# Performance work log

Hardware: AMD Instinct MI355X
Metric: run time of the kernel (lower is better)

Reference implementation:

```python
import jax, jax.numpy as jnp
import numpy as np

SEQ_LEN = 4096
HID = 2048      # hidden_dim == input_dim
NF = 512        # n_features


def setup_inputs() -> dict:
    key = jax.random.key(0)
    ks = jax.random.split(key, 13)
    s = 0.02
    return {
        "x": jax.random.normal(ks[0], (1, 1, NF), jnp.float32),
        "input_hidden": jax.random.normal(ks[1], (1, 1, HID), jnp.float32),
        "input_cell": jax.random.normal(ks[2], (1, 1, HID), jnp.float32),
        "encoder_outputs": jax.random.normal(ks[3], (1, SEQ_LEN, HID), jnp.float32),
        # Bahdanau attention params: Linear(2H -> H) and scoring vector v
        "W_attn": jax.random.normal(ks[4], (HID, 2 * HID), jnp.float32) * s,
        "b_attn": jnp.zeros((HID,), jnp.float32),
        "v_attn": jax.random.normal(ks[5], (HID,), jnp.float32) * s,
        # LSTM params (PyTorch layout, gate order i,f,g,o), input size = H + NF
        "W_ih": jax.random.normal(ks[6], (4 * HID, HID + NF), jnp.float32) * s,
        "W_hh": jax.random.normal(ks[7], (4 * HID, HID), jnp.float32) * s,
        "b_ih": jnp.zeros((4 * HID,), jnp.float32),
        "b_hh": jnp.zeros((4 * HID,), jnp.float32),
        # output Linear(2H -> NF)
        "W_out": jax.random.normal(ks[8], (NF, 2 * HID), jnp.float32) * s,
        "b_out": jnp.zeros((NF,), jnp.float32),
    }


def reference(x, input_hidden, input_cell, encoder_outputs,
              W_attn, b_attn, v_attn, W_ih, W_hh, b_ih, b_hh, W_out, b_out):
    # ---- attention(input_hidden, encoder_outputs) -> a: [B, S] ----
    h_last = input_hidden[-1]                      # [B, H]
    B, S, H = encoder_outputs.shape
    h_rep = jnp.broadcast_to(h_last[:, None, :], (B, S, H))
    energy = jnp.tanh(jnp.concatenate([h_rep, encoder_outputs], axis=-1) @ W_attn.T + b_attn)
    scores = jnp.einsum('bsh,h->bs', energy, v_attn)
    a = jax.nn.softmax(scores, axis=1)             # [B, S]

    # weighted = bmm(a.unsqueeze(1), encoder_outputs) -> [B, H]
    weighted = jnp.einsum('bs,bsh->bh', a, encoder_outputs)

    # ---- single-step LSTM (num_layers=1, batch_first) ----
    rnn_in = jnp.concatenate([x.reshape(1, -1), weighted], axis=-1)  # [1, NF+H]
    h0 = input_hidden[0]                           # [1, H]
    c0 = input_cell[0]                             # [1, H]
    gates = rnn_in @ W_ih.T + b_ih + h0 @ W_hh.T + b_hh  # [1, 4H]
    i, f, g, o = jnp.split(gates, 4, axis=-1)
    c_n = jax.nn.sigmoid(f) * c0 + jax.nn.sigmoid(i) * jnp.tanh(g)
    h_n = jax.nn.sigmoid(o) * jnp.tanh(c_n)        # [1, H] == output.squeeze(0)

    # ---- output projection on cat(output, weighted) ----
    out = jnp.concatenate([h_n, weighted], axis=-1) @ W_out.T + b_out  # [1, NF]
    return out, h_n[None], c_n[None]
```

## Files before the change

kernel.cpp:

```cpp
#include <hip/hip_runtime.h>
#include <hip/hip_bf16.h>
#include <math.h>


#define HIDDEN 2048
#define SEQL   4096
#define NFEAT  512

typedef __attribute__((ext_vector_type(8))) short frag_t;
typedef __attribute__((ext_vector_type(8))) unsigned short u16x8;
typedef __attribute__((ext_vector_type(4))) float f32x4;

__device__ __forceinline__ unsigned short f2bf(float f) {
    union { float f; unsigned int u; } c; c.f = f;
    unsigned int r = c.u + 0x7fffu + ((c.u >> 16) & 1u);
    return (unsigned short)(r >> 16);
}

__device__ __forceinline__ float bf2f(unsigned short u) {
    union { unsigned int u; float f; } c; c.u = (unsigned int)u << 16;
    return c.f;
}

__device__ __forceinline__ float wave_sum(float s) {
    #pragma unroll
    for (int off = 32; off; off >>= 1) s += __shfl_down(s, off);
    return s;
}

__device__ __forceinline__ void gload16(const unsigned short* g, unsigned short* l) {
    __builtin_amdgcn_global_load_lds(
        (const __attribute__((address_space(1))) unsigned int*)g,
        (__attribute__((address_space(3))) unsigned int*)l, 16, 0, 0);
}

__global__ __launch_bounds__(256)
void k_conv_hpre(const float* __restrict__ enc, const float* __restrict__ Wattn,
                 const float* __restrict__ b_attn, const float* __restrict__ h0,
                 unsigned short* __restrict__ encbf, unsigned short* __restrict__ wbf,
                 float* __restrict__ h_pre)
{
    const int b = blockIdx.x;
    if (b < 6144) {
        const float* src;
        unsigned short* dst;
        if (b < 4096) {
            src = enc + (size_t)b * 2048;
            dst = encbf + (size_t)b * 2048;
        } else {
            const int r = b - 4096;
            src = Wattn + (size_t)r * 4096 + 2048;
            dst = wbf + (size_t)r * 2048;
        }
        const int t = threadIdx.x;
        float4 a = *reinterpret_cast<const float4*>(src + t * 8);
        float4 c = *reinterpret_cast<const float4*>(src + t * 8 + 4);
        u16x8 o;
        o[0] = f2bf(a.x); o[1] = f2bf(a.y); o[2] = f2bf(a.z); o[3] = f2bf(a.w);
        o[4] = f2bf(c.x); o[5] = f2bf(c.y); o[6] = f2bf(c.z); o[7] = f2bf(c.w);
        *reinterpret_cast<u16x8*>(dst + t * 8) = o;
    } else {
        const int gw = (b - 6144) * 4 + (threadIdx.x >> 6);
        const int lane = threadIdx.x & 63;
        const float* Wr = Wattn + (size_t)gw * 4096;
        float s = 0.f;
        #pragma unroll
        for (int i = 0; i < 8; i++) {
            int c = i * 256 + lane * 4;
            float4 wv = *reinterpret_cast<const float4*>(Wr + c);
            float4 hv = *reinterpret_cast<const float4*>(h0 + c);
            s += wv.x*hv.x + wv.y*hv.y + wv.z*hv.z + wv.w*hv.w;
        }
        s = wave_sum(s);
        if (lane == 0) h_pre[gw] = s + b_attn[gw];
    }
}

__global__ __launch_bounds__(256)
void k_energy_gates(const unsigned short* __restrict__ encbf,
                    const unsigned short* __restrict__ wbf,
                    const float* __restrict__ h_pre, const float* __restrict__ v_attn,
                    const float* __restrict__ Wih,  const float* __restrict__ Whh,
                    const float* __restrict__ b_ih, const float* __restrict__ b_hh,
                    const float* __restrict__ x,    const float* __restrict__ h0,
                    float* __restrict__ pscore, float* __restrict__ gates)
{
    __shared__ __align__(16) unsigned short As[128 * 64];
    __shared__ __align__(16) unsigned short Bs[128 * 64];
    __shared__ float sh_hv[2][128];
    __shared__ float sh_part[2][128];

    const int tid = threadIdx.x;
    const int wv = tid >> 6, lane = tid & 63;

    if (blockIdx.x >= 512) {
        const int g = blockIdx.x - 512;
        #pragma unroll
        for (int r = 0; r < 2; r++) {
            const int j = g * 8 + wv * 2 + r;
            const float* W1 = Wih + (size_t)j * 2560;
            const float* W2 = Whh + (size_t)j * 2048;
            float s = 0.f;
            #pragma unroll
            for (int i = 0; i < 2; i++) {
                int c = i * 256 + lane * 4;
                float4 wvv = *reinterpret_cast<const float4*>(W1 + c);
                float4 xv = *reinterpret_cast<const float4*>(x + c);
                s += wvv.x*xv.x + wvv.y*xv.y + wvv.z*xv.z + wvv.w*xv.w;
            }
            #pragma unroll
            for (int i = 0; i < 8; i++) {
                int c = i * 256 + lane * 4;
                float4 wvv = *reinterpret_cast<const float4*>(W2 + c);
                float4 hv = *reinterpret_cast<const float4*>(h0 + c);
                s += wvv.x*hv.x + wvv.y*hv.y + wvv.z*hv.z + wvv.w*hv.w;
            }
            s = wave_sum(s);
            if (lane == 0) gates[j] = s + b_ih[j] + b_hh[j];
        }
        return;
    }

    const int hb = blockIdx.x & 15;
    const int sb = blockIdx.x >> 4;
    const int s0 = sb * 128, h0i = hb * 128;
    const int wm = wv >> 1, wn = wv & 1;

    const unsigned short* srcA[4];
    const unsigned short* srcB[4];
    #pragma unroll
    for (int i = 0; i < 4; i++) {
        const int c = wv * 4 + i;
        const int row = c * 8 + (lane >> 3);
        const int k0 = ((lane & 7) ^ (row & 7)) * 8;
        srcA[i] = encbf + (size_t)(s0 + row) * 2048 + k0;
        srcB[i] = wbf  + (size_t)(h0i + row) * 2048 + k0;
    }

    f32x4 acc[4][4];
    #pragma unroll
    for (int m = 0; m < 4; m++)
        #pragma unroll
        for (int n = 0; n < 4; n++)
            acc[m][n] = (f32x4){0.f, 0.f, 0.f, 0.f};

    const int swz = (lane & 7) << 4;
    const int hi16 = (lane >> 4) * 16;

    for (int kt = 0; kt < 2048; kt += 64) {
        __syncthreads();
        #pragma unroll
        for (int i = 0; i < 4; i++) {
            const int c = wv * 4 + i;
            gload16(srcA[i] + kt, &As[c * 512]);
            gload16(srcB[i] + kt, &Bs[c * 512]);
        }
        __syncthreads();

        frag_t af[2][4], bq[2][4];
        #pragma unroll
        for (int ks = 0; ks < 2; ks++) {
            const int lo = (ks * 64 + hi16) ^ swz;
            #pragma unroll
            for (int m = 0; m < 4; m++) {
                const int rowa = wm * 64 + m * 16 + (lane & 15);
                af[ks][m] = *reinterpret_cast<const frag_t*>(
                    reinterpret_cast<const char*>(As) + rowa * 128 + lo);
                const int rowb = wn * 64 + m * 16 + (lane & 15);
                bq[ks][m] = *reinterpret_cast<const frag_t*>(
                    reinterpret_cast<const char*>(Bs) + rowb * 128 + lo);
            }
        }
        #pragma unroll
        for (int ks = 0; ks < 2; ks++)
            #pragma unroll
            for (int m = 0; m < 4; m++)
                #pragma unroll
                for (int n = 0; n < 4; n++)
                    acc[m][n] = __builtin_amdgcn_mfma_f32_16x16x32_bf16(
                        af[ks][m], bq[ks][n], acc[m][n], 0, 0, 0);
    }

    if (tid < 128) { sh_hv[0][tid] = h_pre[h0i + tid]; sh_hv[1][tid] = v_attn[h0i + tid]; }
    __syncthreads();

    float ps[4][4];
    #pragma unroll
    for (int m = 0; m < 4; m++)
        #pragma unroll
        for (int r = 0; r < 4; r++) ps[m][r] = 0.f;

    #pragma unroll
    for (int m = 0; m < 4; m++) {
        #pragma unroll
        for (int n = 0; n < 4; n++) {
            const int hc = wn * 64 + n * 16 + (lane & 15);
            const float hp = sh_hv[0][hc], vvv = sh_hv[1][hc];
            #pragma unroll
            for (int r = 0; r < 4; r++) {
                float e = tanhf(acc[m][n][r] + hp);
                ps[m][r] += e * vvv;
            }
        }
    }
    #pragma unroll
    for (int m = 0; m < 4; m++)
        #pragma unroll
        for (int r = 0; r < 4; r++) {
            float p = ps[m][r];
            #pragma unroll
            for (int off = 1; off < 16; off <<= 1) p += __shfl_xor(p, off);
            ps[m][r] = p;
        }
    if ((lane & 15) == 0) {
        const int grp = lane >> 4;
        #pragma unroll
        for (int m = 0; m < 4; m++)
            #pragma unroll
            for (int r = 0; r < 4; r++)
                sh_part[wn][wm * 64 + m * 16 + grp * 4 + r] = ps[m][r];
    }
    __syncthreads();
    if (tid < 128)
        pscore[hb * SEQL + s0 + tid] = sh_part[0][tid] + sh_part[1][tid];
}

__global__ __launch_bounds__(1024)
void k_softmax(const float* __restrict__ pscore, float* __restrict__ attnw)
{
    __shared__ float red[16];
    __shared__ float bcast;
    const int t = threadIdx.x, wv = t >> 6, lane = t & 63;
    float s[4];
    #pragma unroll
    for (int q = 0; q < 4; q++) {
        const int idx = q * 1024 + t;
        float a = 0.f;
        #pragma unroll
        for (int p = 0; p < 16; p++) a += pscore[p * SEQL + idx];
        s[q] = a;
    }
    float mx = fmaxf(fmaxf(s[0], s[1]), fmaxf(s[2], s[3]));
    #pragma unroll
    for (int off = 32; off; off >>= 1) mx = fmaxf(mx, __shfl_xor(mx, off));
    if (!lane) red[wv] = mx;
    __syncthreads();
    if (t == 0) {
        float m = red[0];
        for (int i = 1; i < 16; i++) m = fmaxf(m, red[i]);
        bcast = m;
    }
    __syncthreads();
    const float bm = bcast;
    float e[4], sum = 0.f;
    #pragma unroll
    for (int q = 0; q < 4; q++) { e[q] = __expf(s[q] - bm); sum += e[q]; }
    #pragma unroll
    for (int off = 32; off; off >>= 1) sum += __shfl_xor(sum, off);
    __syncthreads();
    if (!lane) red[wv] = sum;
    __syncthreads();
    if (t == 0) {
        float m = 0.f;
        for (int i = 0; i < 16; i++) m += red[i];
        bcast = m;
    }
    __syncthreads();
    const float inv = 1.f / bcast;
    #pragma unroll
    for (int q = 0; q < 4; q++) attnw[q * 1024 + t] = e[q] * inv;
}

__global__ __launch_bounds__(256)
void k_weighted_part(const unsigned short* __restrict__ encbf,
                     const float* __restrict__ attnw, float* __restrict__ pweight)
{
    const int blk = blockIdx.x;
    const int t = threadIdx.x;
    const int sbase = blk * 16;
    float acc[8];
    #pragma unroll
    for (int i = 0; i < 8; i++) acc[i] = 0.f;
    for (int s = 0; s < 16; s++) {
        const float a = attnw[sbase + s];
        u16x8 v = *reinterpret_cast<const u16x8*>(encbf + (size_t)(sbase + s) * 2048 + t * 8);
        #pragma unroll
        for (int i = 0; i < 8; i++) acc[i] += a * bf2f(v[i]);
    }
    #pragma unroll
    for (int i = 0; i < 8; i++)
        pweight[(size_t)blk * 2048 + t * 8 + i] = acc[i];
}

__global__ __launch_bounds__(256)
void k_weighted_reduce(const float* __restrict__ pweight, float* __restrict__ weighted)
{
    const int h = blockIdx.x * 256 + threadIdx.x;
    float acc = 0.f;
    #pragma unroll 8
    for (int p = 0; p < 256; p++) acc += pweight[(size_t)p * 2048 + h];
    weighted[h] = acc;
}

__global__ __launch_bounds__(256)
void k_gates_lstm_outR(const float* __restrict__ Wih, const float* __restrict__ weighted,
                       const float* __restrict__ gates, const float* __restrict__ c0,
                       const float* __restrict__ Wout, const float* __restrict__ b_out,
                       float* __restrict__ dout)
{
    __shared__ float sh[4];
    const int wv = threadIdx.x >> 6, lane = threadIdx.x & 63;
    if (blockIdx.x < 2048) {
        const int t = blockIdx.x;
        const int j = t + 2048 * wv;
        const float* Wr = Wih + (size_t)j * 2560 + 512;
        float s = 0.f;
        #pragma unroll
        for (int i = 0; i < 8; i++) {
            int c = i * 256 + lane * 4;
            float4 wvv = *reinterpret_cast<const float4*>(Wr + c);
            float4 hv = *reinterpret_cast<const float4*>(weighted + c);
            s += wvv.x*hv.x + wvv.y*hv.y + wvv.z*hv.z + wvv.w*hv.w;
        }
        s = wave_sum(s);
        if (lane == 0) sh[wv] = s + gates[j];
        __syncthreads();
        if (threadIdx.x == 0) {
            const float gi = sh[0], gf = sh[1], gg = sh[2], go = sh[3];
            const float si = 1.f / (1.f + __expf(-gi));
            const float sf = 1.f / (1.f + __expf(-gf));
            const float so = 1.f / (1.f + __expf(-go));
            const float c = sf * c0[t] + si * tanhf(gg);
            const float h = so * tanhf(c);
            dout[512 + t]  = h;
            dout[2560 + t] = c;
        }
    } else {
        const int n = (blockIdx.x - 2048) * 4 + wv;
        const float* Wr = Wout + (size_t)n * 4096 + 2048;
        float s = 0.f;
        #pragma unroll
        for (int i = 0; i < 8; i++) {
            int c = i * 256 + lane * 4;
            float4 wvv = *reinterpret_cast<const float4*>(Wr + c);
            float4 hv = *reinterpret_cast<const float4*>(weighted + c);
            s += wvv.x*hv.x + wvv.y*hv.y + wvv.z*hv.z + wvv.w*hv.w;
        }
        s = wave_sum(s);
        if (lane == 0) dout[n] = s + b_out[n];
    }
}

__global__ __launch_bounds__(256)
void k_out_left(const float* __restrict__ Wout, const float* __restrict__ hn,
                float* __restrict__ dout)
{
    const int n = (blockIdx.x * 256 + threadIdx.x) >> 6;
    const int lane = threadIdx.x & 63;
    const float* Wr = Wout + (size_t)n * 4096;
    float s = 0.f;
    #pragma unroll
    for (int i = 0; i < 8; i++) {
        int c = i * 256 + lane * 4;
        float4 wv = *reinterpret_cast<const float4*>(Wr + c);
        float4 hv = *reinterpret_cast<const float4*>(hn + c);
        s += wv.x*hv.x + wv.y*hv.y + wv.z*hv.z + wv.w*hv.w;
    }
    s = wave_sum(s);
    if (lane == 0) dout[n] += s;
}

extern "C" void kernel_launch(void* const* d_in, const int* in_sizes, int n_in,
                              void* d_out, int out_size, void* d_ws, size_t ws_size,
                              hipStream_t stream)
{
    const float* x        = (const float*)d_in[0];
    const float* ih       = (const float*)d_in[1];
    const float* ic       = (const float*)d_in[2];
    const float* enc      = (const float*)d_in[3];
    const float* Wattn    = (const float*)d_in[4];
    const float* b_attn   = (const float*)d_in[5];
    const float* v_attn   = (const float*)d_in[6];
    const float* Wih      = (const float*)d_in[7];
    const float* Whh      = (const float*)d_in[8];
    const float* b_ih     = (const float*)d_in[9];
    const float* b_hh     = (const float*)d_in[10];
    const float* Wout     = (const float*)d_in[11];
    const float* b_out    = (const float*)d_in[12];
    float* dout = (float*)d_out;

    unsigned short* encbf = (unsigned short*)d_ws;
    unsigned short* wbf   = encbf + (size_t)8388608;
    float* pweight  = (float*)wbf;
    float* wsf      = (float*)(wbf + (size_t)4194304);
    float* h_pre    = wsf;
    float* gates    = wsf + 2048;
    float* pscore   = wsf + 10240;
    float* attnw    = wsf + 75776;
    float* weighted = wsf + 79872;

    k_conv_hpre<<<6656, 256, 0, stream>>>(enc, Wattn, b_attn, ih, encbf, wbf, h_pre);
    k_energy_gates<<<1536, 256, 0, stream>>>(encbf, wbf, h_pre, v_attn,
                                             Wih, Whh, b_ih, b_hh, x, ih,
                                             pscore, gates);
    k_softmax<<<1, 1024, 0, stream>>>(pscore, attnw);
    k_weighted_part<<<256, 256, 0, stream>>>(encbf, attnw, pweight);
    k_weighted_reduce<<<8, 256, 0, stream>>>(pweight, weighted);
    k_gates_lstm_outR<<<2176, 256, 0, stream>>>(Wih, weighted, gates, ic,
                                                Wout, b_out, dout);
    k_out_left<<<128, 256, 0, stream>>>(Wout, dout + 512, dout);
}
```

Baseline: 110.1 us.

## Shrink energy GEMM tiles, interleave gate blocks, widen weighted-sum reduction

The energy GEMM tile drops from 128x128 to 64x128 along the sequence, so 1024 GEMM blocks run instead of 512, and the W_ih/W_hh gate GEMV blocks are interleaved with them by odd/even block index instead of trailing at the end. The weighted-sum partial kernel now uses 512 blocks of 8 rows. The reduce kernel spreads work over 64 blocks with 8 lanes per output, combined by shuffles, where before 8 blocks looped serially over 256 partials. The goal is better CU occupancy and overlap on the GPU, at the cost of more B-tile reloads per GEMM block and a larger partial buffer.

```diff
diff --git a/kernel.cpp b/kernel.cpp
--- a/kernel.cpp
+++ b/kernel.cpp
@@ -85,16 +85,16 @@
                     const float* __restrict__ x,    const float* __restrict__ h0,
                     float* __restrict__ pscore, float* __restrict__ gates)
 {
-    __shared__ __align__(16) unsigned short As[128 * 64];
+    __shared__ __align__(16) unsigned short As[64 * 64];
     __shared__ __align__(16) unsigned short Bs[128 * 64];
     __shared__ float sh_hv[2][128];
-    __shared__ float sh_part[2][128];
+    __shared__ float sh_part[2][64];
 
     const int tid = threadIdx.x;
     const int wv = tid >> 6, lane = tid & 63;
 
-    if (blockIdx.x >= 512) {
-        const int g = blockIdx.x - 512;
+    if (blockIdx.x & 1) {
+        const int g = blockIdx.x >> 1;
         #pragma unroll
         for (int r = 0; r < 2; r++) {
             const int j = g * 8 + wv * 2 + r;
@@ -121,25 +121,33 @@
         return;
     }
 
-    const int hb = blockIdx.x & 15;
-    const int sb = blockIdx.x >> 4;
-    const int s0 = sb * 128, h0i = hb * 128;
+    const int e = blockIdx.x >> 1;
+    const int hb = e & 15, sb = e >> 4;
+    const int s0 = sb * 64, h0i = hb * 128;
     const int wm = wv >> 1, wn = wv & 1;
 
-    const unsigned short* srcA[4];
-    const unsigned short* srcB[4];
-    #pragma unroll
-    for (int i = 0; i < 4; i++) {
-        const int c = wv * 4 + i;
-        const int row = c * 8 + (lane >> 3);
-        const int k0 = ((lane & 7) ^ (row & 7)) * 8;
-        srcA[i] = encbf + (size_t)(s0 + row) * 2048 + k0;
-        srcB[i] = wbf  + (size_t)(h0i + row) * 2048 + k0;
-    }
-
-    f32x4 acc[4][4];
-    #pragma unroll
-    for (int m = 0; m < 4; m++)
+    const unsigned short* srcP[6];
+    unsigned short* dstP[6];
+    #pragma unroll
+    for (int i = 0; i < 6; i++) {
+        const int c = wv * 6 + i;
+        if (c < 8) {
+            const int row = c * 8 + (lane >> 3);
+            const int k0 = ((lane & 7) ^ (row & 7)) * 8;
+            srcP[i] = encbf + (size_t)(s0 + row) * 2048 + k0;
+            dstP[i] = &As[c * 512];
+        } else {
+            const int cc = c - 8;
+            const int row = cc * 8 + (lane >> 3);
+            const int k0 = ((lane & 7) ^ (row & 7)) * 8;
+            srcP[i] = wbf + (size_t)(h0i + row) * 2048 + k0;
+            dstP[i] = &Bs[cc * 512];
+        }
+    }
+
+    f32x4 acc[2][4];
+    #pragma unroll
+    for (int m = 0; m < 2; m++)
         #pragma unroll
         for (int n = 0; n < 4; n++)
             acc[m][n] = (f32x4){0.f, 0.f, 0.f, 0.f};
@@ -150,31 +158,31 @@
     for (int kt = 0; kt < 2048; kt += 64) {
         __syncthreads();
         #pragma unroll
-        for (int i = 0; i < 4; i++) {
-            const int c = wv * 4 + i;
-            gload16(srcA[i] + kt, &As[c * 512]);
-            gload16(srcB[i] + kt, &Bs[c * 512]);
-        }
+        for (int i = 0; i < 6; i++)
+            gload16(srcP[i] + kt, dstP[i]);
         __syncthreads();
 
-        frag_t af[2][4], bq[2][4];
+        frag_t af[2][2], bq[2][4];
         #pragma unroll
         for (int ks = 0; ks < 2; ks++) {
             const int lo = (ks * 64 + hi16) ^ swz;
             #pragma unroll
-            for (int m = 0; m < 4; m++) {
-                const int rowa = wm * 64 + m * 16 + (lane & 15);
+            for (int m = 0; m < 2; m++) {
+                const int rowa = wm * 32 + m * 16 + (lane & 15);
                 af[ks][m] = *reinterpret_cast<const frag_t*>(
                     reinterpret_cast<const char*>(As) + rowa * 128 + lo);
-                const int rowb = wn * 64 + m * 16 + (lane & 15);
-                bq[ks][m] = *reinterpret_cast<const frag_t*>(
+            }
+            #pragma unroll
+            for (int n = 0; n < 4; n++) {
+                const int rowb = wn * 64 + n * 16 + (lane & 15);
+                bq[ks][n] = *reinterpret_cast<const frag_t*>(
                     reinterpret_cast<const char*>(Bs) + rowb * 128 + lo);
             }
         }
         #pragma unroll
         for (int ks = 0; ks < 2; ks++)
             #pragma unroll
-            for (int m = 0; m < 4; m++)
+            for (int m = 0; m < 2; m++)
                 #pragma unroll
                 for (int n = 0; n < 4; n++)
                     acc[m][n] = __builtin_amdgcn_mfma_f32_16x16x32_bf16(
@@ -184,27 +192,27 @@
     if (tid < 128) { sh_hv[0][tid] = h_pre[h0i + tid]; sh_hv[1][tid] = v_attn[h0i + tid]; }
     __syncthreads();
 
-    float ps[4][4];
-    #pragma unroll
-    for (int m = 0; m < 4; m++)
+    float ps[2][4];
+    #pragma unroll
+    for (int m = 0; m < 2; m++)
         #pragma unroll
         for (int r = 0; r < 4; r++) ps[m][r] = 0.f;
 
     #pragma unroll
-    for (int m = 0; m < 4; m++) {
+    for (int m = 0; m < 2; m++) {
         #pragma unroll
         for (int n = 0; n < 4; n++) {
             const int hc = wn * 64 + n * 16 + (lane & 15);
             const float hp = sh_hv[0][hc], vvv = sh_hv[1][hc];
             #pragma unroll
             for (int r = 0; r < 4; r++) {
-                float e = tanhf(acc[m][n][r] + hp);
-                ps[m][r] += e * vvv;
+                float en = tanhf(acc[m][n][r] + hp);
+                ps[m][r] += en * vvv;
             }
         }
     }
     #pragma unroll
-    for (int m = 0; m < 4; m++)
+    for (int m = 0; m < 2; m++)
         #pragma unroll
         for (int r = 0; r < 4; r++) {
             float p = ps[m][r];
@@ -215,13 +223,13 @@
     if ((lane & 15) == 0) {
         const int grp = lane >> 4;
         #pragma unroll
-        for (int m = 0; m < 4; m++)
+        for (int m = 0; m < 2; m++)
             #pragma unroll
             for (int r = 0; r < 4; r++)
-                sh_part[wn][wm * 64 + m * 16 + grp * 4 + r] = ps[m][r];
-    }
-    __syncthreads();
-    if (tid < 128)
+                sh_part[wn][wm * 32 + m * 16 + grp * 4 + r] = ps[m][r];
+    }
+    __syncthreads();
+    if (tid < 64)
         pscore[hb * SEQL + s0 + tid] = sh_part[0][tid] + sh_part[1][tid];
 }
 
@@ -277,11 +285,12 @@
 {
     const int blk = blockIdx.x;
     const int t = threadIdx.x;
-    const int sbase = blk * 16;
+    const int sbase = blk * 8;
     float acc[8];
     #pragma unroll
     for (int i = 0; i < 8; i++) acc[i] = 0.f;
-    for (int s = 0; s < 16; s++) {
+    #pragma unroll
+    for (int s = 0; s < 8; s++) {
         const float a = attnw[sbase + s];
         u16x8 v = *reinterpret_cast<const u16x8*>(encbf + (size_t)(sbase + s) * 2048 + t * 8);
         #pragma unroll
@@ -295,11 +304,16 @@
 __global__ __launch_bounds__(256)
 void k_weighted_reduce(const float* __restrict__ pweight, float* __restrict__ weighted)
 {
-    const int h = blockIdx.x * 256 + threadIdx.x;
+    const int t = threadIdx.x;
+    const int h = blockIdx.x * 32 + (t >> 3);
+    const int slot = t & 7;
     float acc = 0.f;
     #pragma unroll 8
-    for (int p = 0; p < 256; p++) acc += pweight[(size_t)p * 2048 + h];
-    weighted[h] = acc;
+    for (int p = slot; p < 512; p += 8) acc += pweight[(size_t)p * 2048 + h];
+    acc += __shfl_down(acc, 4);
+    acc += __shfl_down(acc, 2);
+    acc += __shfl_down(acc, 1);
+    if (slot == 0) weighted[h] = acc;
 }
 
 __global__ __launch_bounds__(256)
@@ -400,12 +414,12 @@
     float* weighted = wsf + 79872;
 
     k_conv_hpre<<<6656, 256, 0, stream>>>(enc, Wattn, b_attn, ih, encbf, wbf, h_pre);
-    k_energy_gates<<<1536, 256, 0, stream>>>(encbf, wbf, h_pre, v_attn,
+    k_energy_gates<<<2048, 256, 0, stream>>>(encbf, wbf, h_pre, v_attn,
                                              Wih, Whh, b_ih, b_hh, x, ih,
                                              pscore, gates);
     k_softmax<<<1, 1024, 0, stream>>>(pscore, attnw);
-    k_weighted_part<<<256, 256, 0, stream>>>(encbf, attnw, pweight);
-    k_weighted_reduce<<<8, 256, 0, stream>>>(pweight, weighted);
+    k_weighted_part<<<512, 256, 0, stream>>>(encbf, attnw, pweight);
+    k_weighted_reduce<<<64, 256, 0, stream>>>(pweight, weighted);
     k_gates_lstm_outR<<<2176, 256, 0, stream>>>(Wih, weighted, gates, ic,
                                                 Wout, b_out, dout);
     k_out_left<<<128, 256, 0, stream>>>(Wout, dout + 512, dout);
```

Result: slower. 140.9 us (+27.9%).

## Move LSTM gate GEMV into conversion kernel and widen weighted-sum reduction

Applied to the files above, without the earlier changes.

The h0/x gate GEMV blocks move out of the MFMA energy kernel and into the bf16 conversion kernel, one row per wave, so the energy GEMM grid holds only tiled work. The weighted-sum partial kernel now uses 512 blocks of 8 rows instead of 256 of 16. The reduce kernel uses 64 blocks with 8 lanes per output and a shuffle reduction, where it previously had 8 blocks of serial 256-term sums. The aim is better parallelism in these small latency-bound stages. The cost is more partial-sum traffic through pweight (512 rows).

```diff
diff --git a/kernel.cpp b/kernel.cpp
--- a/kernel.cpp
+++ b/kernel.cpp
@@ -35,10 +35,13 @@
 }
 
 __global__ __launch_bounds__(256)
-void k_conv_hpre(const float* __restrict__ enc, const float* __restrict__ Wattn,
-                 const float* __restrict__ b_attn, const float* __restrict__ h0,
-                 unsigned short* __restrict__ encbf, unsigned short* __restrict__ wbf,
-                 float* __restrict__ h_pre)
+void k_conv_hpre_gates(const float* __restrict__ enc, const float* __restrict__ Wattn,
+                       const float* __restrict__ b_attn, const float* __restrict__ h0,
+                       const float* __restrict__ Wih,  const float* __restrict__ Whh,
+                       const float* __restrict__ b_ih, const float* __restrict__ b_hh,
+                       const float* __restrict__ x,
+                       unsigned short* __restrict__ encbf, unsigned short* __restrict__ wbf,
+                       float* __restrict__ h_pre, float* __restrict__ gates)
 {
     const int b = blockIdx.x;
     if (b < 6144) {
@@ -59,7 +62,7 @@
         o[0] = f2bf(a.x); o[1] = f2bf(a.y); o[2] = f2bf(a.z); o[3] = f2bf(a.w);
         o[4] = f2bf(c.x); o[5] = f2bf(c.y); o[6] = f2bf(c.z); o[7] = f2bf(c.w);
         *reinterpret_cast<u16x8*>(dst + t * 8) = o;
-    } else {
+    } else if (b < 6656) {
         const int gw = (b - 6144) * 4 + (threadIdx.x >> 6);
         const int lane = threadIdx.x & 63;
         const float* Wr = Wattn + (size_t)gw * 4096;
@@ -73,17 +76,36 @@
         }
         s = wave_sum(s);
         if (lane == 0) h_pre[gw] = s + b_attn[gw];
-    }
-}
-
-__global__ __launch_bounds__(256)
-void k_energy_gates(const unsigned short* __restrict__ encbf,
-                    const unsigned short* __restrict__ wbf,
-                    const float* __restrict__ h_pre, const float* __restrict__ v_attn,
-                    const float* __restrict__ Wih,  const float* __restrict__ Whh,
-                    const float* __restrict__ b_ih, const float* __restrict__ b_hh,
-                    const float* __restrict__ x,    const float* __restrict__ h0,
-                    float* __restrict__ pscore, float* __restrict__ gates)
+    } else {
+        const int j = (b - 6656) * 4 + (threadIdx.x >> 6);
+        const int lane = threadIdx.x & 63;
+        const float* W1 = Wih + (size_t)j * 2560;
+        const float* W2 = Whh + (size_t)j * 2048;
+        float s = 0.f;
+        #pragma unroll
+        for (int i = 0; i < 2; i++) {
+            int c = i * 256 + lane * 4;
+            float4 wv = *reinterpret_cast<const float4*>(W1 + c);
+            float4 xv = *reinterpret_cast<const float4*>(x + c);
+            s += wv.x*xv.x + wv.y*xv.y + wv.z*xv.z + wv.w*xv.w;
+        }
+        #pragma unroll
+        for (int i = 0; i < 8; i++) {
+            int c = i * 256 + lane * 4;
+            float4 wv = *reinterpret_cast<const float4*>(W2 + c);
+            float4 hv = *reinterpret_cast<const float4*>(h0 + c);
+            s += wv.x*hv.x + wv.y*hv.y + wv.z*hv.z + wv.w*hv.w;
+        }
+        s = wave_sum(s);
+        if (lane == 0) gates[j] = s + b_ih[j] + b_hh[j];
+    }
+}
+
+__global__ __launch_bounds__(256)
+void k_energy2(const unsigned short* __restrict__ encbf,
+               const unsigned short* __restrict__ wbf,
+               const float* __restrict__ h_pre, const float* __restrict__ v_attn,
+               float* __restrict__ pscore)
 {
     __shared__ __align__(16) unsigned short As[128 * 64];
     __shared__ __align__(16) unsigned short Bs[128 * 64];
@@ -91,39 +113,10 @@
     __shared__ float sh_part[2][128];
 
     const int tid = threadIdx.x;
-    const int wv = tid >> 6, lane = tid & 63;
-
-    if (blockIdx.x >= 512) {
-        const int g = blockIdx.x - 512;
-        #pragma unroll
-        for (int r = 0; r < 2; r++) {
-            const int j = g * 8 + wv * 2 + r;
-            const float* W1 = Wih + (size_t)j * 2560;
-            const float* W2 = Whh + (size_t)j * 2048;
-            float s = 0.f;
-            #pragma unroll
-            for (int i = 0; i < 2; i++) {
-                int c = i * 256 + lane * 4;
-                float4 wvv = *reinterpret_cast<const float4*>(W1 + c);
-                float4 xv = *reinterpret_cast<const float4*>(x + c);
-                s += wvv.x*xv.x + wvv.y*xv.y + wvv.z*xv.z + wvv.w*xv.w;
-            }
-            #pragma unroll
-            for (int i = 0; i < 8; i++) {
-                int c = i * 256 + lane * 4;
-                float4 wvv = *reinterpret_cast<const float4*>(W2 + c);
-                float4 hv = *reinterpret_cast<const float4*>(h0 + c);
-                s += wvv.x*hv.x + wvv.y*hv.y + wvv.z*hv.z + wvv.w*hv.w;
-            }
-            s = wave_sum(s);
-            if (lane == 0) gates[j] = s + b_ih[j] + b_hh[j];
-        }
-        return;
-    }
-
     const int hb = blockIdx.x & 15;
     const int sb = blockIdx.x >> 4;
-    const int s0 = sb * 128, h0i = hb * 128;
+    const int s0 = sb * 128, h0 = hb * 128;
+    const int wv = tid >> 6, lane = tid & 63;
     const int wm = wv >> 1, wn = wv & 1;
 
     const unsigned short* srcA[4];
@@ -134,7 +127,7 @@
         const int row = c * 8 + (lane >> 3);
         const int k0 = ((lane & 7) ^ (row & 7)) * 8;
         srcA[i] = encbf + (size_t)(s0 + row) * 2048 + k0;
-        srcB[i] = wbf  + (size_t)(h0i + row) * 2048 + k0;
+        srcB[i] = wbf  + (size_t)(h0 + row) * 2048 + k0;
     }
 
     f32x4 acc[4][4];
@@ -181,7 +174,7 @@
                         af[ks][m], bq[ks][n], acc[m][n], 0, 0, 0);
     }
 
-    if (tid < 128) { sh_hv[0][tid] = h_pre[h0i + tid]; sh_hv[1][tid] = v_attn[h0i + tid]; }
+    if (tid < 128) { sh_hv[0][tid] = h_pre[h0 + tid]; sh_hv[1][tid] = v_attn[h0 + tid]; }
     __syncthreads();
 
     float ps[4][4];
@@ -277,11 +270,12 @@
 {
     const int blk = blockIdx.x;
     const int t = threadIdx.x;
-    const int sbase = blk * 16;
+    const int sbase = blk * 8;
     float acc[8];
     #pragma unroll
     for (int i = 0; i < 8; i++) acc[i] = 0.f;
-    for (int s = 0; s < 16; s++) {
+    #pragma unroll
+    for (int s = 0; s < 8; s++) {
         const float a = attnw[sbase + s];
         u16x8 v = *reinterpret_cast<const u16x8*>(encbf + (size_t)(sbase + s) * 2048 + t * 8);
         #pragma unroll
@@ -295,11 +289,16 @@
 __global__ __launch_bounds__(256)
 void k_weighted_reduce(const float* __restrict__ pweight, float* __restrict__ weighted)
 {
-    const int h = blockIdx.x * 256 + threadIdx.x;
+    const int t = threadIdx.x;
+    const int h = blockIdx.x * 32 + (t >> 3);
+    const int slot = t & 7;
     float acc = 0.f;
     #pragma unroll 8
-    for (int p = 0; p < 256; p++) acc += pweight[(size_t)p * 2048 + h];
-    weighted[h] = acc;
+    for (int p = slot; p < 512; p += 8) acc += pweight[(size_t)p * 2048 + h];
+    acc += __shfl_down(acc, 4);
+    acc += __shfl_down(acc, 2);
+    acc += __shfl_down(acc, 1);
+    if (slot == 0) weighted[h] = acc;
 }
 
 __global__ __launch_bounds__(256)
@@ -399,13 +398,13 @@
     float* attnw    = wsf + 75776;
     float* weighted = wsf + 79872;
 
-    k_conv_hpre<<<6656, 256, 0, stream>>>(enc, Wattn, b_attn, ih, encbf, wbf, h_pre);
-    k_energy_gates<<<1536, 256, 0, stream>>>(encbf, wbf, h_pre, v_attn,
-                                             Wih, Whh, b_ih, b_hh, x, ih,
-                                             pscore, gates);
+    k_conv_hpre_gates<<<8704, 256, 0, stream>>>(enc, Wattn, b_attn, ih,
+                                                Wih, Whh, b_ih, b_hh, x,
+                                                encbf, wbf, h_pre, gates);
+    k_energy2<<<512, 256, 0, stream>>>(encbf, wbf, h_pre, v_attn, pscore);
     k_softmax<<<1, 1024, 0, stream>>>(pscore, attnw);
-    k_weighted_part<<<256, 256, 0, stream>>>(encbf, attnw, pweight);
-    k_weighted_reduce<<<8, 256, 0, stream>>>(pweight, weighted);
+    k_weighted_part<<<512, 256, 0, stream>>>(encbf, attnw, pweight);
+    k_weighted_reduce<<<64, 256, 0, stream>>>(pweight, weighted);
     k_gates_lstm_outR<<<2176, 256, 0, stream>>>(Wih, weighted, gates, ic,
                                                 Wout, b_out, dout);
     k_out_left<<<128, 256, 0, stream>>>(Wout, dout + 512, dout);
```

Result: no change. 108.0 us (-1.9%).
